# Kernel tuning notes

Hardware: AMD Instinct MI355X
Metric: run time of the kernel (lower is better)

Reference implementation:

```python
import jax, jax.numpy as jnp
import numpy as np
import math

NUM_BUCKETS = 32
MAX_DISTANCE = 128
N_HEADS = 16
D_KV = 64
D_MODEL = 1024


def _relative_position_bucket(relative_position, num_buckets=NUM_BUCKETS, max_distance=MAX_DISTANCE):
    # bidirectional (encoder) variant
    num_buckets = num_buckets // 2
    relative_buckets = (relative_position > 0).astype(jnp.int32) * num_buckets
    relative_position = jnp.abs(relative_position)
    max_exact = num_buckets // 2
    is_small = relative_position < max_exact
    # avoid log(0); masked by is_small anyway
    rp = jnp.maximum(relative_position, 1).astype(jnp.float32)
    rel_if_large = max_exact + (
        jnp.log(rp / max_exact) / math.log(max_distance / max_exact) * (num_buckets - max_exact)
    ).astype(jnp.int32)
    rel_if_large = jnp.minimum(rel_if_large, num_buckets - 1)
    relative_buckets = relative_buckets + jnp.where(is_small, relative_position, rel_if_large)
    return relative_buckets


def compute_bias(rel_bias, q_len, k_len):
    context = jnp.arange(q_len, dtype=jnp.int32)[:, None]
    memory = jnp.arange(k_len, dtype=jnp.int32)[None, :]
    buckets = _relative_position_bucket(memory - context)  # [q,k]
    values = rel_bias[buckets]                              # [q,k,H]
    return jnp.transpose(values, (2, 0, 1))[None]           # [1,H,q,k]


def setup_inputs() -> dict:
    key = jax.random.key(0)
    k1, k2, k3, k4 = jax.random.split(key, 4)
    B, S = 2, 2048
    hidden_states = jax.random.normal(k1, (B, S, D_MODEL), dtype=jnp.float32)
    attention_mask = jnp.ones((B, S), dtype=jnp.int32)
    w_qkv = jax.random.normal(k2, (3 * D_MODEL, D_MODEL), dtype=jnp.float32) * 0.02
    rel_bias = jax.random.normal(k3, (NUM_BUCKETS, N_HEADS), dtype=jnp.float32)
    w_o = jax.random.normal(k4, (D_MODEL, D_MODEL), dtype=jnp.float32) * 0.02
    return {"hidden_states": hidden_states, "attention_mask": attention_mask,
            "w_qkv": w_qkv, "rel_bias": rel_bias, "w_o": w_o}


def reference(hidden_states, attention_mask, w_qkv, rel_bias, w_o):
    B, S, _ = hidden_states.shape
    n, c = N_HEADS, D_KV
    qkv = hidden_states @ w_qkv.T                      # [B,S,3*inner]
    q, k, v = jnp.split(qkv, 3, axis=-1)
    q = q.reshape(B, S, n, c)
    k = k.reshape(B, S, n, c)
    v = v.reshape(B, S, n, c)
    attn_bias = jnp.broadcast_to(compute_bias(rel_bias, S, S), (B, n, S, S))
    mask = attention_mask.reshape(B, 1, 1, S)
    mask_val = jnp.finfo(q.dtype).min
    attn_bias = jnp.where(mask == 0, mask_val, attn_bias)
    attn = jnp.einsum('binc,bjnc->bnij', q, k) + attn_bias   # no 1/sqrt(d) scale in T5
    attn = jax.nn.softmax(attn.astype(jnp.float32), axis=-1).astype(q.dtype)
    x = jnp.einsum('bnij,bjnc->binc', attn, v)
    x = x.reshape(B, S, n * c)
    return x @ w_o.T
```

## Files before the change

### kernel.cpp

```cpp
#include <hip/hip_runtime.h>
#include <stdint.h>

typedef __attribute__((ext_vector_type(4))) float f32x4;
typedef __attribute__((ext_vector_type(8))) short short8;
typedef __attribute__((ext_vector_type(4))) short short4v;
typedef __attribute__((ext_vector_type(2))) unsigned uint2v;

__device__ __forceinline__ short f2bf(float f) {
    union { float f; unsigned u; } x; x.f = f;
    return (short)((x.u + 0x7fffu + ((x.u >> 16) & 1u)) >> 16);
}

__device__ __forceinline__ unsigned cvt_pk_bf16(float lo, float hi) {
    unsigned r;
    asm("v_cvt_pk_bf16_f32 %0, %1, %2" : "=v"(r) : "v"(lo), "v"(hi));
    return r;
}

__device__ __forceinline__ float fexp2(float x) {
#if __has_builtin(__builtin_amdgcn_exp2f)
    return __builtin_amdgcn_exp2f(x);
#else
    return exp2f(x);
#endif
}

#define MFMA16(a, b, c) __builtin_amdgcn_mfma_f32_16x16x32_bf16((a), (b), (c), 0, 0, 0)

__device__ __forceinline__ void gload16(const void* g, void* l) {
    __builtin_amdgcn_global_load_lds((const __attribute__((address_space(1))) void*)g,
                                     (__attribute__((address_space(3))) void*)l, 16, 0, 0);
}

__global__ __launch_bounds__(256) void cast_all(const float* __restrict__ h,
                                                const float* __restrict__ wq,
                                                const float* __restrict__ wo,
                                                short* __restrict__ hb,
                                                short* __restrict__ wqb,
                                                short* __restrict__ wob) {
    int i = blockIdx.x * 256 + threadIdx.x;
    const float* s;
    short* d;
    int j;
    if (i < 524288) { s = h; d = hb; j = i; }
    else if (i < 917504) { s = wq; d = wqb; j = i - 524288; }
    else { s = wo; d = wob; j = i - 917504; }
    float4 a = ((const float4*)s)[j * 2];
    float4 b = ((const float4*)s)[j * 2 + 1];
    short8 o;
    o[0] = f2bf(a.x); o[1] = f2bf(a.y); o[2] = f2bf(a.z); o[3] = f2bf(a.w);
    o[4] = f2bf(b.x); o[5] = f2bf(b.y); o[6] = f2bf(b.z); o[7] = f2bf(b.w);
    ((short8*)d)[j] = o;
}

template <int OUT_BF16, int QSCALE>
__global__ __launch_bounds__(512, 2) void gemm8p(const short* __restrict__ A,
                                                 const short* __restrict__ B,
                                                 void* __restrict__ Cout,
                                                 int M, int N, int K) {
    __shared__ short lds[2][4][8192];
    const int t = threadIdx.x;
    const int l = t & 63, w = t >> 6;
    const int lr = l & 15, lg = l >> 4;
    const int wr = w >> 2, wc = w & 3;
    const int m0 = blockIdx.y * 256, n0 = blockIdx.x * 256;
    const int nt = K >> 6, nh = nt << 2;

    const int sr0 = t >> 2;
    const int scc = ((t & 3) ^ ((sr0 >> 1) & 3)) * 8;
    const short* As0 = A + (size_t)(m0 + sr0) * K + scc;
    const short* As1 = A + (size_t)(m0 + sr0 + 128) * K + scc;
    const short* Bs0 = B + (size_t)(n0 + sr0) * K + scc;
    const short* Bs1 = B + (size_t)(n0 + sr0 + 128) * K + scc;
    short* ldsb = &lds[0][0][0];

    auto stageH = [&](int H) {
        int Tp = H >> 2, pos = H & 3;
        int kb = Tp * 64 + ((pos <= 1) ? 32 : 0);
        short* dst = ldsb + ((Tp & 1) * 4 + pos) * 8192 + t * 8;
        if (pos & 1) {
            gload16(As0 + kb, dst);
            gload16(As1 + kb, dst + 4096);
        } else {
            gload16(Bs0 + kb, dst);
            gload16(Bs1 + kb, dst + 4096);
        }
    };

    int aoff[8], boff[4];
    #pragma unroll
    for (int mi = 0; mi < 8; ++mi) {
        int row = wr * 128 + mi * 16 + lr;
        aoff[mi] = row * 32 + (lg ^ ((row >> 1) & 3)) * 8;
    }
    #pragma unroll
    for (int ni = 0; ni < 4; ++ni) {
        int row = wc * 64 + ni * 16 + lr;
        boff[ni] = row * 32 + (lg ^ ((row >> 1) & 3)) * 8;
    }

    f32x4 acc[8][4] = {};

    for (int H = 0; H < 7; ++H) stageH(H);
    asm volatile("s_waitcnt vmcnt(6)" ::: "memory");
    __builtin_amdgcn_s_barrier();

    for (int T = 0; T < nt; ++T) {
        const short* rbase = ldsb + (T & 1) * 32768;
        const short* B1b = rbase;
        const short* A1b = rbase + 8192;
        const short* B0b = rbase + 16384;
        const short* A0b = rbase + 24576;
        const int Hs = (T << 2) + 7;
        short8 a[4], b[4];

        #pragma unroll
        for (int i = 0; i < 4; ++i) a[i] = *(const short8*)(A1b + aoff[i]);
        #pragma unroll
        for (int i = 0; i < 4; ++i) b[i] = *(const short8*)(B1b + boff[i]);
        if (Hs < nh) stageH(Hs);
        __builtin_amdgcn_sched_barrier(0);
        __builtin_amdgcn_s_barrier();
        asm volatile("s_waitcnt lgkmcnt(0)" ::: "memory");
        __builtin_amdgcn_sched_barrier(0);
        __builtin_amdgcn_s_setprio(1);
        #pragma unroll
        for (int mi = 0; mi < 4; ++mi)
            #pragma unroll
            for (int ni = 0; ni < 4; ++ni)
                acc[mi][ni] = MFMA16(a[mi], b[ni], acc[mi][ni]);
        __builtin_amdgcn_s_setprio(0);
        __builtin_amdgcn_sched_barrier(0);
        __builtin_amdgcn_s_barrier();

        #pragma unroll
        for (int i = 0; i < 4; ++i) a[i] = *(const short8*)(A1b + aoff[4 + i]);
        if (Hs + 1 < nh) stageH(Hs + 1);
        __builtin_amdgcn_sched_barrier(0);
        __builtin_amdgcn_s_barrier();
        asm volatile("s_waitcnt lgkmcnt(0)" ::: "memory");
        __builtin_amdgcn_sched_barrier(0);
        __builtin_amdgcn_s_setprio(1);
        #pragma unroll
        for (int mi = 0; mi < 4; ++mi)
            #pragma unroll
            for (int ni = 0; ni < 4; ++ni)
                acc[4 + mi][ni] = MFMA16(a[mi], b[ni], acc[4 + mi][ni]);
        __builtin_amdgcn_s_setprio(0);
        __builtin_amdgcn_sched_barrier(0);
        __builtin_amdgcn_s_barrier();

        #pragma unroll
        for (int i = 0; i < 4; ++i) a[i] = *(const short8*)(A0b + aoff[i]);
        #pragma unroll
        for (int i = 0; i < 4; ++i) b[i] = *(const short8*)(B0b + boff[i]);
        if (Hs + 2 < nh) stageH(Hs + 2);
        __builtin_amdgcn_sched_barrier(0);
        __builtin_amdgcn_s_barrier();
        asm volatile("s_waitcnt lgkmcnt(0)" ::: "memory");
        __builtin_amdgcn_sched_barrier(0);
        __builtin_amdgcn_s_setprio(1);
        #pragma unroll
        for (int mi = 0; mi < 4; ++mi)
            #pragma unroll
            for (int ni = 0; ni < 4; ++ni)
                acc[mi][ni] = MFMA16(a[mi], b[ni], acc[mi][ni]);
        __builtin_amdgcn_s_setprio(0);
        __builtin_amdgcn_sched_barrier(0);
        __builtin_amdgcn_s_barrier();

        #pragma unroll
        for (int i = 0; i < 4; ++i) a[i] = *(const short8*)(A0b + aoff[4 + i]);
        if (Hs + 3 < nh) stageH(Hs + 3);
        __builtin_amdgcn_sched_barrier(0);
        __builtin_amdgcn_s_barrier();
        asm volatile("s_waitcnt lgkmcnt(0)" ::: "memory");
        __builtin_amdgcn_sched_barrier(0);
        __builtin_amdgcn_s_setprio(1);
        #pragma unroll
        for (int mi = 0; mi < 4; ++mi)
            #pragma unroll
            for (int ni = 0; ni < 4; ++ni)
                acc[4 + mi][ni] = MFMA16(a[mi], b[ni], acc[4 + mi][ni]);
        __builtin_amdgcn_s_setprio(0);
        if (T < nt - 2) {
            asm volatile("s_waitcnt vmcnt(6)" ::: "memory");
        } else if (T == nt - 2) {
            asm volatile("s_waitcnt vmcnt(0)" ::: "memory");
        }
        __builtin_amdgcn_sched_barrier(0);
        __builtin_amdgcn_s_barrier();
    }

    const float qs = (QSCALE && n0 < 1024) ? 1.4426950408889634f : 1.0f;
    #pragma unroll
    for (int mi = 0; mi < 8; ++mi)
        #pragma unroll
        for (int ni = 0; ni < 4; ++ni)
            #pragma unroll
            for (int rr = 0; rr < 4; ++rr) {
                int mm = m0 + wr * 128 + mi * 16 + lg * 4 + rr;
                int nn = n0 + wc * 64 + ni * 16 + lr;
                float v = acc[mi][ni][rr] * qs;
                if (OUT_BF16) ((short*)Cout)[(size_t)mm * N + nn] = f2bf(v);
                else ((float*)Cout)[(size_t)mm * N + nn] = v;
            }
}

template <int OUT_BF16, int QSCALE>
__global__ __launch_bounds__(256) void gemm_bt(const short* __restrict__ A,
                                               const short* __restrict__ B,
                                               void* __restrict__ Cout,
                                               int M, int N, int K) {
    __shared__ short sA[4096];
    __shared__ short sB[4096];
    const int t = threadIdx.x;
    const int l = t & 63, w = t >> 6;
    const int lr = l & 15, lg = l >> 4;
    const int m0 = blockIdx.y * 128, n0 = blockIdx.x * 128;
    const int wm = (w >> 1) * 64, wn = (w & 1) * 64;
    const int c0 = w * 64 + l, c1 = c0 + 256;
    const short* Ap0 = A + (size_t)(m0 + (c0 >> 2)) * K + (c0 & 3) * 8;
    const short* Ap1 = A + (size_t)(m0 + (c1 >> 2)) * K + (c1 & 3) * 8;
    const short* Bp0 = B + (size_t)(n0 + (c0 >> 2)) * K + (c0 & 3) * 8;
    const short* Bp1 = B + (size_t)(n0 + (c1 >> 2)) * K + (c1 & 3) * 8;
    short* lA0 = sA + w * 512;
    short* lA1 = sA + 2048 + w * 512;
    short* lB0 = sB + w * 512;
    short* lB1 = sB + 2048 + w * 512;
    f32x4 acc[4][4] = {};
    for (int k0 = 0; k0 < K; k0 += 32) {
        gload16(Ap0 + k0, lA0);
        gload16(Ap1 + k0, lA1);
        gload16(Bp0 + k0, lB0);
        gload16(Bp1 + k0, lB1);
        __syncthreads();
        short8 af[4], bfr[4];
        #pragma unroll
        for (int m = 0; m < 4; ++m) af[m] = *(const short8*)&sA[(wm + m * 16 + lr) * 32 + lg * 8];
        #pragma unroll
        for (int n = 0; n < 4; ++n) bfr[n] = *(const short8*)&sB[(wn + n * 16 + lr) * 32 + lg * 8];
        #pragma unroll
        for (int m = 0; m < 4; ++m)
            #pragma unroll
            for (int n = 0; n < 4; ++n)
                acc[m][n] = MFMA16(af[m], bfr[n], acc[m][n]);
        __syncthreads();
    }
    const float qs = (QSCALE && n0 < 1024) ? 1.4426950408889634f : 1.0f;
    #pragma unroll
    for (int m = 0; m < 4; ++m)
        #pragma unroll
        for (int n = 0; n < 4; ++n)
            #pragma unroll
            for (int r = 0; r < 4; ++r) {
                int mm = m0 + wm + m * 16 + lg * 4 + r;
                int nn = n0 + wn + n * 16 + lr;
                float v = acc[m][n][r] * qs;
                if (OUT_BF16) ((short*)Cout)[(size_t)mm * N + nn] = f2bf(v);
                else ((float*)Cout)[(size_t)mm * N + nn] = v;
            }
}

__global__ __launch_bounds__(256) void transpose_v(const short* __restrict__ qkv,
                                                   short* __restrict__ vt) {
    __shared__ short T[64][72];
    const int t = threadIdx.x;
    const int s0 = blockIdx.x * 64, bh = blockIdx.y;
    const int b = bh >> 4, h = bh & 15;
    const int rl = t >> 2, cg = (t & 3) * 16;
    const short* src = qkv + (size_t)(b * 2048 + s0 + rl) * 3072 + 2048 + h * 64 + cg;
    *(short8*)&T[rl][cg] = *(const short8*)src;
    *(short8*)&T[rl][cg + 8] = *(const short8*)(src + 8);
    __syncthreads();
    short8 o0, o1;
    #pragma unroll
    for (int e = 0; e < 8; ++e) o0[e] = T[cg + e][rl];
    #pragma unroll
    for (int e = 0; e < 8; ++e) o1[e] = T[cg + 8 + e][rl];
    short* dst = vt + ((size_t)bh * 64 + rl) * 2048 + s0 + cg;
    *(short8*)dst = o0;
    *(short8*)(dst + 8) = o1;
}

__global__ __launch_bounds__(512, 4) void attn_kernel(const short* __restrict__ qkv,
                                                      const short* __restrict__ vt,
                                                      const int* __restrict__ amask,
                                                      const float* __restrict__ rel_bias,
                                                      short* __restrict__ xout) {
    __shared__ float tbl[340];
    __shared__ short sK[2][4096];
    __shared__ short sV[2][4096];
    __shared__ short sP[8][16][72];
    __shared__ int mflags[32];
    const int t = threadIdx.x;
    const int l = t & 63, w = t >> 6;
    const int lr = l & 15, lg = l >> 4;
    const int qt = blockIdx.x, bh = blockIdx.y;
    const int b = bh >> 4, h = bh & 15;
    const int q0 = qt * 128 + w * 16;
    const float LOG2E = 1.4426950408889634f;

    if (t < 32) mflags[t] = ~0;
    if (t < 337) {
        int idx = t;
        int d = idx - 168;
        int a = d < 0 ? -d : d;
        int fb = a < 8 ? a
                 : (a < 12 ? 8 : a < 16 ? 9 : a < 23 ? 10 : a < 32 ? 11
                    : a < 46 ? 12 : a < 64 ? 13 : a < 91 ? 14 : 15);
        int bk = (d > 0 ? 16 : 0) + fb;
        tbl[idx] = rel_bias[bk * 16 + h] * LOG2E;
    }
    const float rbp = rel_bias[31 * 16 + h] * LOG2E;
    const float rbn = rel_bias[15 * 16 + h] * LOG2E;

    short8 qf[2];
    #pragma unroll
    for (int ds = 0; ds < 2; ++ds)
        qf[ds] = *(const short8*)(qkv + (size_t)(b * 2048 + q0 + lr) * 3072 + h * 64 + ds * 32 + lg * 8);

    const int4 ma = ((const int4*)(amask + b * 2048))[t];

    const int srow = t >> 3;
    const int scp = ((t & 7) ^ (srow & 7)) * 8;
    const short* kgp = qkv + (size_t)(b * 2048 + srow) * 3072 + 1024 + h * 64 + scp;
    const short* vgp = vt + ((size_t)bh * 64 + srow) * 2048 + scp;
    const int sw8 = (lr & 7) * 8;
    const int ibb = -q0 + lg * 4 - lr + 168;

    __syncthreads();
    int mok = ma.x & ma.y & ma.z & ma.w;
    if (mok == 0) atomicAnd(&mflags[t >> 4], 0);
    __syncthreads();

    gload16(kgp, &sK[0][0] + t * 8);
    gload16(vgp, &sV[0][0] + t * 8);

    f32x4 o[4] = {};
    float mreg = -1e30f, lreg = 0.f;

    for (int kt = 0; kt < 2048; kt += 64) {
        const int cur = (kt >> 6) & 1;
        if (kt + 64 < 2048) {
            gload16(kgp + (size_t)(kt + 64) * 3072, &sK[cur ^ 1][0] + t * 8);
            gload16(vgp + kt + 64, &sV[cur ^ 1][0] + t * 8);
            asm volatile("s_waitcnt vmcnt(2)" ::: "memory");
        } else {
            asm volatile("s_waitcnt vmcnt(0)" ::: "memory");
        }
        __builtin_amdgcn_sched_barrier(0);
        __builtin_amdgcn_s_barrier();
        __builtin_amdgcn_sched_barrier(0);

        const short* kb = &sK[cur][0];
        const short* vb = &sV[cur][0];

        f32x4 pe[4];
        #pragma unroll
        for (int ct = 0; ct < 4; ++ct) {
            f32x4 z = {};
            #pragma unroll
            for (int ds = 0; ds < 2; ++ds) {
                short8 kf = *(const short8*)&kb[(ct * 16 + lr) * 64 + ((ds * 32 + lg * 8) ^ sw8)];
                z = MFMA16(kf, qf[ds], z);
            }
            pe[ct] = z;
        }

        float cb;
        if (kt >= q0 + 106) {
            cb = rbp;
        } else if (kt + 63 <= q0 - 91) {
            cb = rbn;
        } else {
            cb = 0.f;
            const int ib = kt + ibb;
            #pragma unroll
            for (int ct = 0; ct < 4; ++ct)
                #pragma unroll
                for (int r = 0; r < 4; ++r)
                    pe[ct][r] += tbl[ib + ct * 16 + r];
        }

        float t0 = fmaxf(fmaxf(pe[0][0], pe[0][1]), fmaxf(pe[0][2], pe[0][3]));
        float t1 = fmaxf(fmaxf(pe[1][0], pe[1][1]), fmaxf(pe[1][2], pe[1][3]));
        float t2 = fmaxf(fmaxf(pe[2][0], pe[2][1]), fmaxf(pe[2][2], pe[2][3]));
        float t3 = fmaxf(fmaxf(pe[3][0], pe[3][1]), fmaxf(pe[3][2], pe[3][3]));
        float lmax = fmaxf(fmaxf(t0, t1), fmaxf(t2, t3));
        if (__any(lmax > mreg - cb + 11.5f)) {
            float rm = fmaxf(lmax, __shfl_xor(lmax, 16));
            rm = fmaxf(rm, __shfl_xor(rm, 32));
            float mnew = fmaxf(mreg, rm + cb);
            float alpha = fexp2(mreg - mnew);
            lreg *= alpha;
            #pragma unroll
            for (int dt = 0; dt < 4; ++dt)
                #pragma unroll
                for (int r = 0; r < 4; ++r)
                    o[dt][r] *= alpha;
            mreg = mnew;
        }
        const float madj = mreg - cb;
        const int tok = mflags[kt >> 6];
        float rs = 0.f;
        if (tok) {
            #pragma unroll
            for (int ct = 0; ct < 4; ++ct) {
                float p[4];
                #pragma unroll
                for (int r = 0; r < 4; ++r) {
                    float pv = fexp2(pe[ct][r] - madj);
                    p[r] = pv;
                    rs += pv;
                }
                uint2v pk;
                pk[0] = cvt_pk_bf16(p[0], p[1]);
                pk[1] = cvt_pk_bf16(p[2], p[3]);
                *(uint2v*)&sP[w][lr][ct * 16 + lg * 4] = pk;
            }
        } else {
            const int4* mp = (const int4*)(amask + b * 2048 + kt);
            #pragma unroll
            for (int ct = 0; ct < 4; ++ct) {
                int4 cm = mp[ct * 4 + lg];
                float p[4];
                #pragma unroll
                for (int r = 0; r < 4; ++r) {
                    float pv = fexp2(pe[ct][r] - madj);
                    pv = ((const int*)&cm)[r] ? pv : 0.f;
                    p[r] = pv;
                    rs += pv;
                }
                uint2v pk;
                pk[0] = cvt_pk_bf16(p[0], p[1]);
                pk[1] = cvt_pk_bf16(p[2], p[3]);
                *(uint2v*)&sP[w][lr][ct * 16 + lg * 4] = pk;
            }
        }
        lreg += rs;

        #pragma unroll
        for (int kk = 0; kk < 2; ++kk) {
            short8 pf = *(const short8*)&sP[w][lr][kk * 32 + lg * 8];
            #pragma unroll
            for (int dt = 0; dt < 4; ++dt) {
                short8 vf = *(const short8*)&vb[(dt * 16 + lr) * 64 + ((kk * 32 + lg * 8) ^ sw8)];
                o[dt] = MFMA16(vf, pf, o[dt]);
            }
        }
        __builtin_amdgcn_sched_barrier(0);
        __builtin_amdgcn_s_barrier();
        __builtin_amdgcn_sched_barrier(0);
    }

    float lsum = lreg + __shfl_xor(lreg, 16);
    lsum += __shfl_xor(lsum, 32);
    const float inv = 1.0f / lsum;
    #pragma unroll
    for (int dt = 0; dt < 4; ++dt) {
        short4v ov;
        #pragma unroll
        for (int r = 0; r < 4; ++r) ov[r] = f2bf(o[dt][r] * inv);
        *(short4v*)(xout + (size_t)(b * 2048 + q0 + lr) * 1024 + h * 64 + dt * 16 + lg * 4) = ov;
    }
}

extern "C" void kernel_launch(void* const* d_in, const int* in_sizes, int n_in,
                              void* d_out, int out_size, void* d_ws, size_t ws_size,
                              hipStream_t stream) {
    const float* hidden = (const float*)d_in[0];
    const int* amask = (const int*)d_in[1];
    const float* w_qkv = (const float*)d_in[2];
    const float* rel_bias = (const float*)d_in[3];
    const float* w_o = (const float*)d_in[4];
    if (ws_size < 58720256) return;
    char* ws = (char*)d_ws;
    short* hidden_bf = (short*)(ws + 0);
    short* wqkv_bf   = (short*)(ws + 8388608);
    short* wo_bf     = (short*)(ws + 14680064);
    short* qkv       = (short*)(ws + 16777216);
    short* vt        = (short*)(ws + 41943040);
    short* xbuf      = (short*)(ws + 50331648);

    cast_all<<<4096, 256, 0, stream>>>(hidden, w_qkv, w_o, hidden_bf, wqkv_bf, wo_bf);
    gemm8p<1, 1><<<dim3(12, 16), 512, 0, stream>>>(hidden_bf, wqkv_bf, qkv, 4096, 3072, 1024);
    transpose_v<<<dim3(32, 32), 256, 0, stream>>>(qkv, vt);
    attn_kernel<<<dim3(16, 32), 512, 0, stream>>>(qkv, vt, amask, rel_bias, xbuf);
    gemm_bt<0, 0><<<dim3(8, 32), 256, 0, stream>>>(xbuf, wo_bf, d_out, 4096, 1024, 1024);
}
```

Baseline: 134.7 us.

## Process two 16-row query chunks per wave to reuse K/V fragments

Each wave in the attention kernel now handles 32 query rows (two 16-row chunks) instead of 16. Each K and V fragment read from shared memory feeds two MFMAs, which halves LDS traffic and global K/V loads per query. The grid shrinks to 256 blocks and the launch-bounds occupancy hint drops to 2, so register pressure rises while parallelism on the 256-CU device falls. The relative-bias table offset and the far-window thresholds are adjusted to cover the larger query span.

New measurement: 142.2 us. 1.06x slower.

```diff
diff --git a/kernel.cpp b/kernel.cpp
--- a/kernel.cpp
+++ b/kernel.cpp
@@ -283,42 +283,44 @@
     *(short8*)(dst + 8) = o1;
 }
 
-__global__ __launch_bounds__(512, 4) void attn_kernel(const short* __restrict__ qkv,
+__global__ __launch_bounds__(512, 2) void attn_kernel(const short* __restrict__ qkv,
                                                       const short* __restrict__ vt,
                                                       const int* __restrict__ amask,
                                                       const float* __restrict__ rel_bias,
                                                       short* __restrict__ xout) {
-    __shared__ float tbl[340];
+    __shared__ float tbl[320];
     __shared__ short sK[2][4096];
     __shared__ short sV[2][4096];
-    __shared__ short sP[8][16][72];
+    __shared__ short sP[8][32][72];
     __shared__ int mflags[32];
     const int t = threadIdx.x;
     const int l = t & 63, w = t >> 6;
     const int lr = l & 15, lg = l >> 4;
     const int qt = blockIdx.x, bh = blockIdx.y;
     const int b = bh >> 4, h = bh & 15;
-    const int q0 = qt * 128 + w * 16;
+    const int q0 = qt * 256 + w * 32;
     const float LOG2E = 1.4426950408889634f;
 
     if (t < 32) mflags[t] = ~0;
-    if (t < 337) {
-        int idx = t;
-        int d = idx - 168;
+    if (t < 319) {
+        int d = t - 159;
         int a = d < 0 ? -d : d;
         int fb = a < 8 ? a
                  : (a < 12 ? 8 : a < 16 ? 9 : a < 23 ? 10 : a < 32 ? 11
                     : a < 46 ? 12 : a < 64 ? 13 : a < 91 ? 14 : 15);
         int bk = (d > 0 ? 16 : 0) + fb;
-        tbl[idx] = rel_bias[bk * 16 + h] * LOG2E;
+        tbl[t] = rel_bias[bk * 16 + h] * LOG2E;
     }
     const float rbp = rel_bias[31 * 16 + h] * LOG2E;
     const float rbn = rel_bias[15 * 16 + h] * LOG2E;
 
-    short8 qf[2];
-    #pragma unroll
-    for (int ds = 0; ds < 2; ++ds)
-        qf[ds] = *(const short8*)(qkv + (size_t)(b * 2048 + q0 + lr) * 3072 + h * 64 + ds * 32 + lg * 8);
+    short8 qf[2][2];
+    #pragma unroll
+    for (int qc = 0; qc < 2; ++qc)
+        #pragma unroll
+        for (int ds = 0; ds < 2; ++ds)
+            qf[qc][ds] = *(const short8*)(qkv + (size_t)(b * 2048 + q0 + qc * 16 + lr) * 3072 +
+                                          h * 64 + ds * 32 + lg * 8);
 
     const int4 ma = ((const int4*)(amask + b * 2048))[t];
 
@@ -327,7 +329,7 @@
     const short* kgp = qkv + (size_t)(b * 2048 + srow) * 3072 + 1024 + h * 64 + scp;
     const short* vgp = vt + ((size_t)bh * 64 + srow) * 2048 + scp;
     const int sw8 = (lr & 7) * 8;
-    const int ibb = -q0 + lg * 4 - lr + 168;
+    const int ibb = -q0 + lg * 4 - lr + 159;
 
     __syncthreads();
     int mok = ma.x & ma.y & ma.z & ma.w;
@@ -337,8 +339,8 @@
     gload16(kgp, &sK[0][0] + t * 8);
     gload16(vgp, &sV[0][0] + t * 8);
 
-    f32x4 o[4] = {};
-    float mreg = -1e30f, lreg = 0.f;
+    f32x4 o[4][2] = {};
+    float mreg[2] = {-1e30f, -1e30f}, lreg[2] = {0.f, 0.f};
 
     for (int kt = 0; kt < 2048; kt += 64) {
         const int cur = (kt >> 6) & 1;
@@ -356,20 +358,22 @@
         const short* kb = &sK[cur][0];
         const short* vb = &sV[cur][0];
 
-        f32x4 pe[4];
+        f32x4 pe[4][2];
         #pragma unroll
         for (int ct = 0; ct < 4; ++ct) {
-            f32x4 z = {};
+            f32x4 z0 = {}, z1 = {};
             #pragma unroll
             for (int ds = 0; ds < 2; ++ds) {
                 short8 kf = *(const short8*)&kb[(ct * 16 + lr) * 64 + ((ds * 32 + lg * 8) ^ sw8)];
-                z = MFMA16(kf, qf[ds], z);
+                z0 = MFMA16(kf, qf[0][ds], z0);
+                z1 = MFMA16(kf, qf[1][ds], z1);
             }
-            pe[ct] = z;
+            pe[ct][0] = z0;
+            pe[ct][1] = z1;
         }
 
         float cb;
-        if (kt >= q0 + 106) {
+        if (kt >= q0 + 122) {
             cb = rbp;
         } else if (kt + 63 <= q0 - 91) {
             cb = rbn;
@@ -377,76 +381,91 @@
             cb = 0.f;
             const int ib = kt + ibb;
             #pragma unroll
-            for (int ct = 0; ct < 4; ++ct)
+            for (int qc = 0; qc < 2; ++qc)
                 #pragma unroll
-                for (int r = 0; r < 4; ++r)
-                    pe[ct][r] += tbl[ib + ct * 16 + r];
-        }
-
-        float t0 = fmaxf(fmaxf(pe[0][0], pe[0][1]), fmaxf(pe[0][2], pe[0][3]));
-        float t1 = fmaxf(fmaxf(pe[1][0], pe[1][1]), fmaxf(pe[1][2], pe[1][3]));
-        float t2 = fmaxf(fmaxf(pe[2][0], pe[2][1]), fmaxf(pe[2][2], pe[2][3]));
-        float t3 = fmaxf(fmaxf(pe[3][0], pe[3][1]), fmaxf(pe[3][2], pe[3][3]));
-        float lmax = fmaxf(fmaxf(t0, t1), fmaxf(t2, t3));
-        if (__any(lmax > mreg - cb + 11.5f)) {
-            float rm = fmaxf(lmax, __shfl_xor(lmax, 16));
-            rm = fmaxf(rm, __shfl_xor(rm, 32));
-            float mnew = fmaxf(mreg, rm + cb);
-            float alpha = fexp2(mreg - mnew);
-            lreg *= alpha;
-            #pragma unroll
-            for (int dt = 0; dt < 4; ++dt)
+                for (int ct = 0; ct < 4; ++ct)
+                    #pragma unroll
+                    for (int r = 0; r < 4; ++r)
+                        pe[ct][qc][r] += tbl[ib - qc * 16 + ct * 16 + r];
+        }
+
+        float lmax[2];
+        #pragma unroll
+        for (int qc = 0; qc < 2; ++qc) {
+            float t0 = fmaxf(fmaxf(pe[0][qc][0], pe[0][qc][1]), fmaxf(pe[0][qc][2], pe[0][qc][3]));
+            float t1 = fmaxf(fmaxf(pe[1][qc][0], pe[1][qc][1]), fmaxf(pe[1][qc][2], pe[1][qc][3]));
+            float t2 = fmaxf(fmaxf(pe[2][qc][0], pe[2][qc][1]), fmaxf(pe[2][qc][2], pe[2][qc][3]));
+            float t3 = fmaxf(fmaxf(pe[3][qc][0], pe[3][qc][1]), fmaxf(pe[3][qc][2], pe[3][qc][3]));
+            lmax[qc] = fmaxf(fmaxf(t0, t1), fmaxf(t2, t3));
+        }
+        bool need = (lmax[0] > mreg[0] - cb + 11.5f) | (lmax[1] > mreg[1] - cb + 11.5f);
+        if (__any(need)) {
+            #pragma unroll
+            for (int qc = 0; qc < 2; ++qc) {
+                float rm = fmaxf(lmax[qc], __shfl_xor(lmax[qc], 16));
+                rm = fmaxf(rm, __shfl_xor(rm, 32));
+                float mnew = fmaxf(mreg[qc], rm + cb);
+                float alpha = fexp2(mreg[qc] - mnew);
+                lreg[qc] *= alpha;
                 #pragma unroll
-                for (int r = 0; r < 4; ++r)
-                    o[dt][r] *= alpha;
-            mreg = mnew;
-        }
-        const float madj = mreg - cb;
+                for (int dt = 0; dt < 4; ++dt)
+                    #pragma unroll
+                    for (int r = 0; r < 4; ++r)
+                        o[dt][qc][r] *= alpha;
+                mreg[qc] = mnew;
+            }
+        }
         const int tok = mflags[kt >> 6];
-        float rs = 0.f;
-        if (tok) {
-            #pragma unroll
-            for (int ct = 0; ct < 4; ++ct) {
-                float p[4];
+        #pragma unroll
+        for (int qc = 0; qc < 2; ++qc) {
+            const float madj = mreg[qc] - cb;
+            float rs = 0.f;
+            if (tok) {
                 #pragma unroll
-                for (int r = 0; r < 4; ++r) {
-                    float pv = fexp2(pe[ct][r] - madj);
-                    p[r] = pv;
-                    rs += pv;
+                for (int ct = 0; ct < 4; ++ct) {
+                    float p[4];
+                    #pragma unroll
+                    for (int r = 0; r < 4; ++r) {
+                        float pv = fexp2(pe[ct][qc][r] - madj);
+                        p[r] = pv;
+                        rs += pv;
+                    }
+                    uint2v pk;
+                    pk[0] = cvt_pk_bf16(p[0], p[1]);
+                    pk[1] = cvt_pk_bf16(p[2], p[3]);
+                    *(uint2v*)&sP[w][qc * 16 + lr][ct * 16 + lg * 4] = pk;
                 }
-                uint2v pk;
-                pk[0] = cvt_pk_bf16(p[0], p[1]);
-                pk[1] = cvt_pk_bf16(p[2], p[3]);
-                *(uint2v*)&sP[w][lr][ct * 16 + lg * 4] = pk;
+            } else {
+                const int4* mp = (const int4*)(amask + b * 2048 + kt);
+                #pragma unroll
+                for (int ct = 0; ct < 4; ++ct) {
+                    int4 cm = mp[ct * 4 + lg];
+                    float p[4];
+                    #pragma unroll
+                    for (int r = 0; r < 4; ++r) {
+                        float pv = fexp2(pe[ct][qc][r] - madj);
+                        pv = ((const int*)&cm)[r] ? pv : 0.f;
+                        p[r] = pv;
+                        rs += pv;
+                    }
+                    uint2v pk;
+                    pk[0] = cvt_pk_bf16(p[0], p[1]);
+                    pk[1] = cvt_pk_bf16(p[2], p[3]);
+                    *(uint2v*)&sP[w][qc * 16 + lr][ct * 16 + lg * 4] = pk;
+                }
             }
-        } else {
-            const int4* mp = (const int4*)(amask + b * 2048 + kt);
-            #pragma unroll
-            for (int ct = 0; ct < 4; ++ct) {
-                int4 cm = mp[ct * 4 + lg];
-                float p[4];
-                #pragma unroll
-                for (int r = 0; r < 4; ++r) {
-                    float pv = fexp2(pe[ct][r] - madj);
-                    pv = ((const int*)&cm)[r] ? pv : 0.f;
-                    p[r] = pv;
-                    rs += pv;
-                }
-                uint2v pk;
-                pk[0] = cvt_pk_bf16(p[0], p[1]);
-                pk[1] = cvt_pk_bf16(p[2], p[3]);
-                *(uint2v*)&sP[w][lr][ct * 16 + lg * 4] = pk;
-            }
-        }
-        lreg += rs;
+            lreg[qc] += rs;
+        }
 
         #pragma unroll
         for (int kk = 0; kk < 2; ++kk) {
-            short8 pf = *(const short8*)&sP[w][lr][kk * 32 + lg * 8];
+            short8 pf0 = *(const short8*)&sP[w][lr][kk * 32 + lg * 8];
+            short8 pf1 = *(const short8*)&sP[w][16 + lr][kk * 32 + lg * 8];
             #pragma unroll
             for (int dt = 0; dt < 4; ++dt) {
                 short8 vf = *(const short8*)&vb[(dt * 16 + lr) * 64 + ((kk * 32 + lg * 8) ^ sw8)];
-                o[dt] = MFMA16(vf, pf, o[dt]);
+                o[dt][0] = MFMA16(vf, pf0, o[dt][0]);
+                o[dt][1] = MFMA16(vf, pf1, o[dt][1]);
             }
         }
         __builtin_amdgcn_sched_barrier(0);
@@ -454,15 +473,19 @@
         __builtin_amdgcn_sched_barrier(0);
     }
 
-    float lsum = lreg + __shfl_xor(lreg, 16);
-    lsum += __shfl_xor(lsum, 32);
-    const float inv = 1.0f / lsum;
-    #pragma unroll
-    for (int dt = 0; dt < 4; ++dt) {
-        short4v ov;
-        #pragma unroll
-        for (int r = 0; r < 4; ++r) ov[r] = f2bf(o[dt][r] * inv);
-        *(short4v*)(xout + (size_t)(b * 2048 + q0 + lr) * 1024 + h * 64 + dt * 16 + lg * 4) = ov;
+    #pragma unroll
+    for (int qc = 0; qc < 2; ++qc) {
+        float lsum = lreg[qc] + __shfl_xor(lreg[qc], 16);
+        lsum += __shfl_xor(lsum, 32);
+        const float inv = 1.0f / lsum;
+        #pragma unroll
+        for (int dt = 0; dt < 4; ++dt) {
+            short4v ov;
+            #pragma unroll
+            for (int r = 0; r < 4; ++r) ov[r] = f2bf(o[dt][qc][r] * inv);
+            *(short4v*)(xout + (size_t)(b * 2048 + q0 + qc * 16 + lr) * 1024 +
+                        h * 64 + dt * 16 + lg * 4) = ov;
+        }
     }
 }
 
@@ -486,6 +509,6 @@
     cast_all<<<4096, 256, 0, stream>>>(hidden, w_qkv, w_o, hidden_bf, wqkv_bf, wo_bf);
     gemm8p<1, 1><<<dim3(12, 16), 512, 0, stream>>>(hidden_bf, wqkv_bf, qkv, 4096, 3072, 1024);
     transpose_v<<<dim3(32, 32), 256, 0, stream>>>(qkv, vt);
-    attn_kernel<<<dim3(16, 32), 512, 0, stream>>>(qkv, vt, amask, rel_bias, xbuf);
+    attn_kernel<<<dim3(8, 32), 512, 0, stream>>>(qkv, vt, amask, rel_bias, xbuf);
     gemm_bt<0, 0><<<dim3(8, 32), 256, 0, stream>>>(xbuf, wo_bf, d_out, 4096, 1024, 1024);
 }
```
